# Performance work log

Measured on AMD Instinct MI355X. Metric: run time of the kernel, lower is better.

The kernel has to match this reference:

```python
import jax, jax.numpy as jnp
import numpy as np

H = W = 56
HID = 384
B = 16

def dct_mat(N):
    # Orthonormal DCT-II matrix: X = D @ x, idct via D.T
    n = jnp.arange(N, dtype=jnp.float32)
    k = jnp.arange(N, dtype=jnp.float32)[:, None]
    D = jnp.cos(jnp.pi * (2.0 * n + 1.0) * k / (2.0 * N)) * jnp.sqrt(2.0 / N)
    D = D.at[0].multiply(1.0 / jnp.sqrt(2.0))
    return D

def setup_inputs() -> dict:
    key = jax.random.key(0)
    ks = jax.random.split(key, 16)
    s = 0.02
    return {
        "x": jax.random.normal(ks[0], (B, HID, H, W), dtype=jnp.float32),
        "freq_embed": jax.random.normal(ks[1], (H, W, HID), dtype=jnp.float32),
        "dw_w": jax.random.normal(ks[2], (HID, 1, 3, 3), dtype=jnp.float32) * s,
        "dw_b": jnp.zeros((HID,), jnp.float32),
        "lin_w": jax.random.normal(ks[3], (2 * HID, HID), dtype=jnp.float32) * s,
        "lin_b": jnp.zeros((2 * HID,), jnp.float32),
        "vel_w": jax.random.normal(ks[4], (HID, HID), dtype=jnp.float32) * s,
        "vel_b": jnp.zeros((HID,), jnp.float32),
        "tok_w": jax.random.normal(ks[5], (HID, HID), dtype=jnp.float32) * s,
        "tok_b": jnp.zeros((HID,), jnp.float32),
        "ln_g": jnp.ones((HID,), jnp.float32),
        "ln_b": jnp.zeros((HID,), jnp.float32),
        "out_w": jax.random.normal(ks[6], (HID, HID), dtype=jnp.float32) * s,
        "out_b": jnp.zeros((HID,), jnp.float32),
        "c": jnp.ones((1,), jnp.float32),
        "alpha": jnp.ones((1,), jnp.float32) * 0.1,
    }

def reference(x, freq_embed, dw_w, dw_b, lin_w, lin_b, vel_w, vel_b,
              tok_w, tok_b, ln_g, ln_b, out_w, out_b, c, alpha):
    Bn, C, Hh, Ww = x.shape
    # depthwise 3x3 conv, padding=1
    x = jax.lax.conv_general_dilated(
        x, dw_w, (1, 1), 'SAME',
        dimension_numbers=('NCHW', 'OIHW', 'NCHW'),
        feature_group_count=C) + dw_b[None, :, None, None]
    xl = jnp.transpose(x, (0, 2, 3, 1))            # [B,H,W,C]
    xz = xl @ lin_w.T + lin_b                      # [B,H,W,2C]
    xg, z = jnp.split(xz, 2, axis=-1)
    DH, DW_ = dct_mat(Hh), dct_mat(Ww)
    x_ch = jnp.transpose(xg, (0, 3, 1, 2))         # [B,C,H,W]
    x_u0 = jnp.einsum('ih,jw,bchw->bcij', DH, DW_, x_ch)
    x_vel = xg @ vel_w.T + vel_b                   # [B,H,W,C]
    x_v0 = jnp.einsum('ih,jw,bchw->bcij', DH, DW_, jnp.transpose(x_vel, (0, 3, 1, 2)))
    # decay map exp(-(n^2+m^2)) on linspace(0,pi)
    wn = jnp.linspace(0.0, jnp.pi, Hh + 1)[:Hh][:, None]
    wm = jnp.linspace(0.0, jnp.pi, Ww + 1)[:Ww][None, :]
    decay = jnp.exp(-(wn ** 2 + wm ** 2))[None, None]
    x_u0 = x_u0 * decay
    x_v0 = x_v0 * decay
    # wave modulation from freq embedding (shared across batch)
    t = jax.nn.relu(freq_embed @ tok_w.T + tok_b)  # [H,W,C]
    t = jnp.transpose(t, (2, 0, 1))[None]          # [1,C,H,W]
    eps = 1e-6
    cos_t = jnp.cos(c[0] * t)
    sin_t = jnp.sin(c[0] * t) / (c[0] + eps)
    final = cos_t * x_u0 + sin_t * (x_v0 + 0.5 * alpha[0] * x_u0)
    x_final = jnp.einsum('hi,wj,bchw->bcij', DH, DW_, final)  # IDCT2D
    y = jnp.transpose(x_final, (0, 2, 3, 1))       # [B,H,W,C]
    mu = jnp.mean(y, axis=-1, keepdims=True)
    var = jnp.mean((y - mu) ** 2, axis=-1, keepdims=True)
    yn = (y - mu) / jnp.sqrt(var + 1e-5) * ln_g + ln_b
    gated = yn * jax.nn.silu(z)                    # [B,H,W,C]
    out = gated @ out_w.T + out_b
    return jnp.transpose(out, (0, 3, 1, 2))        # [B,C,H,W]
```

## Files before the change

### kernel.cpp

```cpp
#include <hip/hip_runtime.h>
#include <math.h>

#define HH 56
#define WS_W 56
#define HWS 3136
#define CD 384
#define BB 16
#define NROW (BB*HWS)
#define SLOT ((size_t)NROW*CD)

typedef __attribute__((ext_vector_type(8))) short bf16x8;
typedef __attribute__((ext_vector_type(4))) float f32x4;

__device__ inline ushort f2bf(float v) {
  uint u = __float_as_uint(v);
  uint r = (u + 0x7fffu + ((u >> 16) & 1u)) >> 16;
  return (ushort)r;
}
__device__ inline float bf2f(ushort h) { return __uint_as_float((uint)h << 16); }

__device__ inline void split_octet(const float* f, uint4& hi, uint4& lo) {
  ushort hs[8], ls[8];
  #pragma unroll
  for (int i = 0; i < 8; ++i) {
    float v = f[i];
    ushort h = f2bf(v);
    hs[i] = h;
    ls[i] = f2bf(v - bf2f(h));
  }
  hi.x = hs[0] | ((uint)hs[1] << 16); hi.y = hs[2] | ((uint)hs[3] << 16);
  hi.z = hs[4] | ((uint)hs[5] << 16); hi.w = hs[6] | ((uint)hs[7] << 16);
  lo.x = ls[0] | ((uint)ls[1] << 16); lo.y = ls[2] | ((uint)ls[3] << 16);
  lo.z = ls[4] | ((uint)ls[5] << 16); lo.w = ls[6] | ((uint)ls[7] << 16);
}

__global__ void prep_d_k(float* __restrict__ D) {
  for (int idx = threadIdx.x; idx < HH*HH; idx += blockDim.x) {
    int k = idx / HH, n = idx % HH;
    double v = cos(3.14159265358979323846 * (2.0*n + 1.0) * k / (2.0*HH)) * sqrt(2.0/HH);
    if (k == 0) v *= 0.70710678118654752440;
    D[idx] = (float)v;
  }
}

__global__ __launch_bounds__(256) void split_w_k(
    const float* __restrict__ W, ushort* __restrict__ hi,
    ushort* __restrict__ lo, int nelem) {
  int i = blockIdx.x*256 + threadIdx.x;
  if (i >= nelem) return;
  float v = W[i];
  ushort h = f2bf(v);
  hi[i] = h;
  lo[i] = f2bf(v - bf2f(h));
}

__global__ __launch_bounds__(256) void conv_k(
    const float* __restrict__ x, const float* __restrict__ dww,
    const float* __restrict__ dwb, float* __restrict__ xc)
{
  __shared__ float xs[3][58][33];
  __shared__ float wgt[32][9];
  __shared__ float wb[32];
  int t = threadIdx.x;
  int c0 = blockIdx.x * 32, h = blockIdx.y, b = blockIdx.z;
  for (int idx = t; idx < 1344; idx += 256) {
    int wq = idx % 14, rem = idx / 14;
    int dy = rem % 3, ch = rem / 3;
    int gh = h + dy - 1;
    float4 v = {0.f, 0.f, 0.f, 0.f};
    if (gh >= 0 && gh < HH)
      v = *(const float4*)(x + (((size_t)b*CD + c0 + ch)*HH + gh)*WS_W + wq*4);
    int wp = wq*4 + 1;
    xs[dy][wp+0][ch] = v.x;
    xs[dy][wp+1][ch] = v.y;
    xs[dy][wp+2][ch] = v.z;
    xs[dy][wp+3][ch] = v.w;
  }
  if (t < 192) {
    int e = t & 1, dy = (t >> 1) % 3, ch = t / 6;
    xs[dy][e*57][ch] = 0.f;
  }
  for (int idx = t; idx < 288; idx += 256)
    wgt[idx/9][idx%9] = dww[(size_t)(c0 + idx/9)*9 + idx%9];
  if (t < 32) wb[t] = dwb[c0 + t];
  __syncthreads();
  int ch = t & 31, wq8 = t >> 5;
  #pragma unroll
  for (int wwi = 0; wwi < 7; ++wwi) {
    int w = wwi*8 + wq8;
    float acc = wb[ch];
    #pragma unroll
    for (int dy = 0; dy < 3; ++dy)
      #pragma unroll
      for (int dx = 0; dx < 3; ++dx)
        acc = fmaf(wgt[ch][dy*3+dx], xs[dy][w+dx][ch], acc);
    xc[((size_t)b*HWS + h*WS_W + w)*CD + c0 + ch] = acc;
  }
}

template<int EPI>
__global__ __launch_bounds__(256) void gemm_k(
    const float* __restrict__ A, const float* __restrict__ Bw,
    const float* __restrict__ bias, float* __restrict__ out0,
    float* __restrict__ out1, const float* __restrict__ cptr)
{
  __shared__ float As[16][68];
  __shared__ float Bs[16][68];
  int t = threadIdx.x;
  int col0 = blockIdx.x * 64;
  int row0 = blockIdx.y * 64;
  int lr = t >> 2, lk = (t & 3) * 4;
  const float* Ap = A + (size_t)(row0 + lr)*CD + lk;
  const float* Bp = Bw + (size_t)(col0 + lr)*CD + lk;
  float acc[4][4] = {};
  int tx = t & 15, ty = t >> 4;
  for (int k0 = 0; k0 < CD; k0 += 16) {
    float4 av = *(const float4*)(Ap + k0);
    float4 bv = *(const float4*)(Bp + k0);
    __syncthreads();
    As[lk+0][lr] = av.x; As[lk+1][lr] = av.y; As[lk+2][lr] = av.z; As[lk+3][lr] = av.w;
    Bs[lk+0][lr] = bv.x; Bs[lk+1][lr] = bv.y; Bs[lk+2][lr] = bv.z; Bs[lk+3][lr] = bv.w;
    __syncthreads();
    #pragma unroll
    for (int k = 0; k < 16; ++k) {
      float4 a4 = *(const float4*)&As[k][ty*4];
      float4 b4 = *(const float4*)&Bs[k][tx*4];
      float aa[4] = {a4.x, a4.y, a4.z, a4.w};
      float bbv[4] = {b4.x, b4.y, b4.z, b4.w};
      #pragma unroll
      for (int i = 0; i < 4; ++i)
        #pragma unroll
        for (int j = 0; j < 4; ++j)
          acc[i][j] = fmaf(aa[i], bbv[j], acc[i][j]);
    }
  }
  float cs = 0.f;
  if constexpr (EPI == 2) cs = cptr[0];
  #pragma unroll
  for (int i = 0; i < 4; ++i) {
    int r = row0 + ty*4 + i;
    #pragma unroll
    for (int j = 0; j < 4; ++j) {
      int cg = col0 + tx*4 + j;
      float v = acc[i][j];
      if constexpr (EPI == 2) {
        v += bias[cg];
        v = fmaxf(v, 0.f);
        int pi = r / 56, pj = r % 56;
        float wn = 3.14159265358979323846f/56.f * (float)pi;
        float wm = 3.14159265358979323846f/56.f * (float)pj;
        float dec = expf(-(wn*wn + wm*wm));
        out0[(size_t)r*CD + cg] = cosf(cs*v)*dec;
        out1[(size_t)r*CD + cg] = sinf(cs*v)/(cs + 1e-6f)*dec;
      }
    }
  }
}

template<int EPI>
__global__ __launch_bounds__(256, 2) void mgemm_k(
    const float* __restrict__ A, const ushort* __restrict__ Wh,
    const ushort* __restrict__ Wl, const float* __restrict__ bias,
    float* __restrict__ out0, float* __restrict__ out1,
    const float* __restrict__ Uin, const float* __restrict__ cosD,
    const float* __restrict__ sinD, const float* __restrict__ velb,
    const float* __restrict__ alphap)
{
  __shared__ char smem[32768];
  int t = threadIdx.x;
  int col0 = blockIdx.x * 128, row0 = blockIdx.y * 128;
  int r = t >> 1, half = t & 1;
  int n = r & 15, rt = r >> 4, q0 = half * 2;
  const float*  Ap  = A  + (size_t)(row0 + r)*CD + half*16;
  const ushort* Bhp = Wh + (size_t)(col0 + r)*CD + half*16;
  const ushort* Blp = Wl + (size_t)(col0 + r)*CD + half*16;
  int aoff0 = rt*1024 + (q0*16 + n)*16;
  int aoff1 = rt*1024 + ((q0+1)*16 + n)*16;
  int boff0 = 16384 + aoff0, boff1 = 16384 + aoff1;
  int wid = t >> 6, lane = t & 63;
  int wr = wid >> 1, wc = wid & 1;
  f32x4 acc[4][4];
  #pragma unroll
  for (int i = 0; i < 4; ++i)
    #pragma unroll
    for (int j = 0; j < 4; ++j)
      acc[i][j] = (f32x4){0.f, 0.f, 0.f, 0.f};

  for (int k0 = 0; k0 < CD; k0 += 32) {
    float4 f0 = *(const float4*)(Ap + k0);
    float4 f1 = *(const float4*)(Ap + k0 + 4);
    float4 f2 = *(const float4*)(Ap + k0 + 8);
    float4 f3 = *(const float4*)(Ap + k0 + 12);
    uint4 bh0 = *(const uint4*)(Bhp + k0);
    uint4 bh1 = *(const uint4*)(Bhp + k0 + 8);
    uint4 bl0 = *(const uint4*)(Blp + k0);
    uint4 bl1 = *(const uint4*)(Blp + k0 + 8);
    __syncthreads();
    float fa[16] = {f0.x,f0.y,f0.z,f0.w, f1.x,f1.y,f1.z,f1.w,
                    f2.x,f2.y,f2.z,f2.w, f3.x,f3.y,f3.z,f3.w};
    uint4 ah0, al0, ah1, al1;
    split_octet(&fa[0], ah0, al0);
    split_octet(&fa[8], ah1, al1);
    *(uint4*)(smem + aoff0)        = ah0;
    *(uint4*)(smem + aoff0 + 8192) = al0;
    *(uint4*)(smem + aoff1)        = ah1;
    *(uint4*)(smem + aoff1 + 8192) = al1;
    *(uint4*)(smem + boff0)        = bh0;
    *(uint4*)(smem + boff0 + 8192) = bl0;
    *(uint4*)(smem + boff1)        = bh1;
    *(uint4*)(smem + boff1 + 8192) = bl1;
    __syncthreads();
    bf16x8 Ah[4], Al[4], Bh[4], Bl[4];
    #pragma unroll
    for (int i = 0; i < 4; ++i) {
      int ao = (wr*4 + i)*1024 + lane*16;
      Ah[i] = *(const bf16x8*)(smem + ao);
      Al[i] = *(const bf16x8*)(smem + ao + 8192);
      int bo = 16384 + (wc*4 + i)*1024 + lane*16;
      Bh[i] = *(const bf16x8*)(smem + bo);
      Bl[i] = *(const bf16x8*)(smem + bo + 8192);
    }
    #pragma unroll
    for (int i = 0; i < 4; ++i)
      #pragma unroll
      for (int j = 0; j < 4; ++j) {
        acc[i][j] = __builtin_amdgcn_mfma_f32_16x16x32_bf16(Ah[i], Bh[j], acc[i][j], 0, 0, 0);
        acc[i][j] = __builtin_amdgcn_mfma_f32_16x16x32_bf16(Ah[i], Bl[j], acc[i][j], 0, 0, 0);
        acc[i][j] = __builtin_amdgcn_mfma_f32_16x16x32_bf16(Al[i], Bh[j], acc[i][j], 0, 0, 0);
      }
  }

  int nn = lane & 15, qq = lane >> 4;
  float ahalf = 0.f;
  if constexpr (EPI == 1) ahalf = 0.5f * alphap[0];
  #pragma unroll
  for (int i = 0; i < 4; ++i) {
    #pragma unroll
    for (int j = 0; j < 4; ++j) {
      #pragma unroll
      for (int reg = 0; reg < 4; ++reg) {
        int rg = row0 + wr*64 + i*16 + qq*4 + reg;
        int cg = col0 + wc*64 + j*16 + nn;
        float v = acc[i][j][reg];
        if constexpr (EPI == 0) {
          v += bias[cg];
          if (cg < CD) out0[(size_t)rg*CD + cg] = v;
          else         out1[(size_t)rg*CD + cg - CD] = v;
        } else if constexpr (EPI == 1) {
          int p = rg % HWS;
          float u  = Uin[(size_t)rg*CD + cg];
          float cd = cosD[(size_t)p*CD + cg];
          float sd = sinD[(size_t)p*CD + cg];
          if (p == 0) v += 56.f * velb[cg];
          out0[(size_t)rg*CD + cg] = cd*u + sd*(v + ahalf*u);
        } else {
          v += bias[cg];
          int bidx = rg / HWS, hw = rg % HWS;
          out0[((size_t)bidx*CD + cg)*HWS + hw] = v;
        }
      }
    }
  }
}

__global__ __launch_bounds__(448) void dct_k(
    const float* __restrict__ in, float* __restrict__ out,
    const float* __restrict__ D, int NC, int trans)
{
  __shared__ float Ds[56][60];
  __shared__ float Xs[56][128];
  int t = threadIdx.x;
  int c0 = blockIdx.x * 128;
  size_t bt = blockIdx.y;
  for (int idx = t; idx < 3136; idx += 448) {
    int k = idx / 56, m = idx % 56;
    Ds[k][m] = trans ? D[k*56 + m] : D[m*56 + k];
  }
  const float* inb = in + bt*56*(size_t)NC + c0;
  for (int fi = t; fi < 56*32; fi += 448) {
    int rw = fi >> 5, cg = fi & 31;
    *(float4*)&Xs[rw][cg*4] = *(const float4*)(inb + (size_t)rw*NC + cg*4);
  }
  __syncthreads();
  int tx = t % 32, ty = t / 32;
  float acc[4][4] = {};
  #pragma unroll 4
  for (int k = 0; k < 56; ++k) {
    float4 a4 = *(const float4*)&Ds[k][ty*4];
    float4 b4 = *(const float4*)&Xs[k][tx*4];
    float aa[4] = {a4.x, a4.y, a4.z, a4.w};
    float bbv[4] = {b4.x, b4.y, b4.z, b4.w};
    #pragma unroll
    for (int i = 0; i < 4; ++i)
      #pragma unroll
      for (int j = 0; j < 4; ++j)
        acc[i][j] = fmaf(aa[i], bbv[j], acc[i][j]);
  }
  float* ob = out + bt*56*(size_t)NC + c0;
  #pragma unroll
  for (int i = 0; i < 4; ++i) {
    int m = ty*4 + i;
    float4 o; o.x = acc[i][0]; o.y = acc[i][1]; o.z = acc[i][2]; o.w = acc[i][3];
    *(float4*)(ob + (size_t)m*NC + tx*4) = o;
  }
}

__global__ __launch_bounds__(256) void ln_gate_k(
    const float* __restrict__ Y, const float* __restrict__ Z,
    const float* __restrict__ g, const float* __restrict__ be,
    float* __restrict__ out)
{
  int lane = threadIdx.x & 63, wv = threadIdx.x >> 6;
  size_t r = (size_t)blockIdx.x*4 + wv;
  const float* y = Y + r*CD;
  float v[6];
  float s = 0.f;
  #pragma unroll
  for (int q = 0; q < 6; ++q) { v[q] = y[lane + 64*q]; s += v[q]; }
  #pragma unroll
  for (int off = 32; off > 0; off >>= 1) s += __shfl_xor(s, off, 64);
  float mu = s * (1.f/384.f);
  float s2 = 0.f;
  #pragma unroll
  for (int q = 0; q < 6; ++q) { float d = v[q]-mu; s2 += d*d; }
  #pragma unroll
  for (int off = 32; off > 0; off >>= 1) s2 += __shfl_xor(s2, off, 64);
  float rs = 1.f / sqrtf(s2*(1.f/384.f) + 1e-5f);
  #pragma unroll
  for (int q = 0; q < 6; ++q) {
    int c = lane + 64*q;
    float yn = (v[q]-mu)*rs*g[c] + be[c];
    float zv = Z[r*CD + c];
    float sz = zv / (1.f + expf(-zv));
    out[r*CD + c] = yn*sz;
  }
}

extern "C" void kernel_launch(void* const* d_in, const int* in_sizes, int n_in,
                              void* d_out, int out_size, void* d_ws, size_t ws_size,
                              hipStream_t stream) {
  const float* x     = (const float*)d_in[0];
  const float* fe    = (const float*)d_in[1];
  const float* dw_w  = (const float*)d_in[2];
  const float* dw_b  = (const float*)d_in[3];
  const float* lin_w = (const float*)d_in[4];
  const float* lin_b = (const float*)d_in[5];
  const float* vel_w = (const float*)d_in[6];
  const float* vel_b = (const float*)d_in[7];
  const float* tok_w = (const float*)d_in[8];
  const float* tok_b = (const float*)d_in[9];
  const float* ln_g  = (const float*)d_in[10];
  const float* ln_b  = (const float*)d_in[11];
  const float* out_w = (const float*)d_in[12];
  const float* out_b = (const float*)d_in[13];
  const float* cp    = (const float*)d_in[14];
  const float* ap    = (const float*)d_in[15];

  float* ws    = (float*)d_ws;
  float* slotA = ws;
  float* slotB = ws + SLOT;
  float* slotC = ws + 2*SLOT;
  float* Dm    = ws + 3*SLOT;
  float* cosD  = Dm + 3136;
  float* sinD  = cosD + (size_t)HWS*CD;
  ushort* whi  = (ushort*)(sinD + (size_t)HWS*CD);
  ushort* wlo  = whi + 589824;

  prep_d_k<<<1, 256, 0, stream>>>(Dm);
  split_w_k<<<1152, 256, 0, stream>>>(lin_w, whi,          wlo,          294912);
  split_w_k<<< 576, 256, 0, stream>>>(vel_w, whi + 294912, wlo + 294912, 147456);
  split_w_k<<< 576, 256, 0, stream>>>(out_w, whi + 442368, wlo + 442368, 147456);

  conv_k<<<dim3(12, 56, 16), 256, 0, stream>>>(x, dw_w, dw_b, slotA);
  gemm_k<2><<<dim3(6, 49), 256, 0, stream>>>(fe, tok_w, tok_b, cosD, sinD, cp);
  mgemm_k<0><<<dim3(6, 392), 256, 0, stream>>>(slotA, whi, wlo, lin_b,
      slotB, slotC, nullptr, nullptr, nullptr, nullptr, nullptr);
  dct_k<<<dim3(168, 16), 448, 0, stream>>>(slotB, slotA, Dm, 21504, 0);
  dct_k<<<dim3(3, 896), 448, 0, stream>>>(slotA, slotB, Dm, 384, 0);
  mgemm_k<1><<<dim3(3, 392), 256, 0, stream>>>(slotB, whi + 294912, wlo + 294912,
      nullptr, slotA, nullptr, slotB, cosD, sinD, vel_b, ap);
  dct_k<<<dim3(168, 16), 448, 0, stream>>>(slotA, slotB, Dm, 21504, 1);
  dct_k<<<dim3(3, 896), 448, 0, stream>>>(slotB, slotA, Dm, 384, 1);
  ln_gate_k<<<12544, 256, 0, stream>>>(slotA, slotC, ln_g, ln_b, slotB);
  mgemm_k<3><<<dim3(3, 392), 256, 0, stream>>>(slotB, whi + 442368, wlo + 442368,
      out_b, (float*)d_out, nullptr, nullptr, nullptr, nullptr, nullptr, nullptr);
}
```

Measured before the change: 749.6 us.

## Emit bf16 hi/lo split activations from producer kernels instead of splitting in GEMM

The conv, second DCT pass and LayerNorm-gate kernels now write activations as pre-split bf16 hi/lo pairs. The MFMA GEMM then loads these directly into shared memory instead of converting fp32 on every K step. This removes redundant split arithmetic from the GEMM inner loop, since each A tile is re-split for every column block. It also raises the occupancy hint from 2 to 3 blocks per SM. Global traffic for A stays about the same (two 16-bit arrays replace one 32-bit array), and the split cost moves into the producer epilogues.

```diff
diff --git a/kernel.cpp b/kernel.cpp
--- a/kernel.cpp
+++ b/kernel.cpp
@@ -18,21 +18,6 @@
   return (ushort)r;
 }
 __device__ inline float bf2f(ushort h) { return __uint_as_float((uint)h << 16); }
-
-__device__ inline void split_octet(const float* f, uint4& hi, uint4& lo) {
-  ushort hs[8], ls[8];
-  #pragma unroll
-  for (int i = 0; i < 8; ++i) {
-    float v = f[i];
-    ushort h = f2bf(v);
-    hs[i] = h;
-    ls[i] = f2bf(v - bf2f(h));
-  }
-  hi.x = hs[0] | ((uint)hs[1] << 16); hi.y = hs[2] | ((uint)hs[3] << 16);
-  hi.z = hs[4] | ((uint)hs[5] << 16); hi.w = hs[6] | ((uint)hs[7] << 16);
-  lo.x = ls[0] | ((uint)ls[1] << 16); lo.y = ls[2] | ((uint)ls[3] << 16);
-  lo.z = ls[4] | ((uint)ls[5] << 16); lo.w = ls[6] | ((uint)ls[7] << 16);
-}
 
 __global__ void prep_d_k(float* __restrict__ D) {
   for (int idx = threadIdx.x; idx < HH*HH; idx += blockDim.x) {
@@ -56,7 +41,8 @@
 
 __global__ __launch_bounds__(256) void conv_k(
     const float* __restrict__ x, const float* __restrict__ dww,
-    const float* __restrict__ dwb, float* __restrict__ xc)
+    const float* __restrict__ dwb, ushort* __restrict__ xcH,
+    ushort* __restrict__ xcL)
 {
   __shared__ float xs[3][58][33];
   __shared__ float wgt[32][9];
@@ -94,7 +80,10 @@
       #pragma unroll
       for (int dx = 0; dx < 3; ++dx)
         acc = fmaf(wgt[ch][dy*3+dx], xs[dy][w+dx][ch], acc);
-    xc[((size_t)b*HWS + h*WS_W + w)*CD + c0 + ch] = acc;
+    size_t oi = ((size_t)b*HWS + h*WS_W + w)*CD + c0 + ch;
+    ushort hh = f2bf(acc);
+    xcH[oi] = hh;
+    xcL[oi] = f2bf(acc - bf2f(hh));
   }
 }
 
@@ -158,25 +147,26 @@
 }
 
 template<int EPI>
-__global__ __launch_bounds__(256, 2) void mgemm_k(
-    const float* __restrict__ A, const ushort* __restrict__ Wh,
-    const ushort* __restrict__ Wl, const float* __restrict__ bias,
+__global__ __launch_bounds__(256, 3) void mgemm_k(
+    const ushort* __restrict__ Ahg, const ushort* __restrict__ Alg,
+    const ushort* __restrict__ Wh, const ushort* __restrict__ Wl,
+    const float* __restrict__ bias,
     float* __restrict__ out0, float* __restrict__ out1,
-    const float* __restrict__ Uin, const float* __restrict__ cosD,
-    const float* __restrict__ sinD, const float* __restrict__ velb,
-    const float* __restrict__ alphap)
+    const ushort* __restrict__ UinH, const ushort* __restrict__ UinL,
+    const float* __restrict__ cosD, const float* __restrict__ sinD,
+    const float* __restrict__ velb, const float* __restrict__ alphap)
 {
   __shared__ char smem[32768];
   int t = threadIdx.x;
   int col0 = blockIdx.x * 128, row0 = blockIdx.y * 128;
   int r = t >> 1, half = t & 1;
-  int n = r & 15, rt = r >> 4, q0 = half * 2;
-  const float*  Ap  = A  + (size_t)(row0 + r)*CD + half*16;
-  const ushort* Bhp = Wh + (size_t)(col0 + r)*CD + half*16;
-  const ushort* Blp = Wl + (size_t)(col0 + r)*CD + half*16;
-  int aoff0 = rt*1024 + (q0*16 + n)*16;
-  int aoff1 = rt*1024 + ((q0+1)*16 + n)*16;
-  int boff0 = 16384 + aoff0, boff1 = 16384 + aoff1;
+  int n = r & 15, st = r >> 4, q0 = half * 2;
+  const ushort* Ahp = Ahg + (size_t)(row0 + r)*CD + half*16;
+  const ushort* Alp = Alg + (size_t)(row0 + r)*CD + half*16;
+  const ushort* Bhp = Wh  + (size_t)(col0 + r)*CD + half*16;
+  const ushort* Blp = Wl  + (size_t)(col0 + r)*CD + half*16;
+  int off0 = st*1024 + (q0*16 + n)*16;
+  int off1 = st*1024 + ((q0+1)*16 + n)*16;
   int wid = t >> 6, lane = t & 63;
   int wr = wid >> 1, wc = wid & 1;
   f32x4 acc[4][4];
@@ -187,28 +177,23 @@
       acc[i][j] = (f32x4){0.f, 0.f, 0.f, 0.f};
 
   for (int k0 = 0; k0 < CD; k0 += 32) {
-    float4 f0 = *(const float4*)(Ap + k0);
-    float4 f1 = *(const float4*)(Ap + k0 + 4);
-    float4 f2 = *(const float4*)(Ap + k0 + 8);
-    float4 f3 = *(const float4*)(Ap + k0 + 12);
-    uint4 bh0 = *(const uint4*)(Bhp + k0);
-    uint4 bh1 = *(const uint4*)(Bhp + k0 + 8);
-    uint4 bl0 = *(const uint4*)(Blp + k0);
-    uint4 bl1 = *(const uint4*)(Blp + k0 + 8);
+    uint4 a0 = *(const uint4*)(Ahp + k0);
+    uint4 a1 = *(const uint4*)(Ahp + k0 + 8);
+    uint4 l0 = *(const uint4*)(Alp + k0);
+    uint4 l1 = *(const uint4*)(Alp + k0 + 8);
+    uint4 b0 = *(const uint4*)(Bhp + k0);
+    uint4 b1 = *(const uint4*)(Bhp + k0 + 8);
+    uint4 c0v = *(const uint4*)(Blp + k0);
+    uint4 c1v = *(const uint4*)(Blp + k0 + 8);
     __syncthreads();
-    float fa[16] = {f0.x,f0.y,f0.z,f0.w, f1.x,f1.y,f1.z,f1.w,
-                    f2.x,f2.y,f2.z,f2.w, f3.x,f3.y,f3.z,f3.w};
-    uint4 ah0, al0, ah1, al1;
-    split_octet(&fa[0], ah0, al0);
-    split_octet(&fa[8], ah1, al1);
-    *(uint4*)(smem + aoff0)        = ah0;
-    *(uint4*)(smem + aoff0 + 8192) = al0;
-    *(uint4*)(smem + aoff1)        = ah1;
-    *(uint4*)(smem + aoff1 + 8192) = al1;
-    *(uint4*)(smem + boff0)        = bh0;
-    *(uint4*)(smem + boff0 + 8192) = bl0;
-    *(uint4*)(smem + boff1)        = bh1;
-    *(uint4*)(smem + boff1 + 8192) = bl1;
+    *(uint4*)(smem + off0)         = a0;
+    *(uint4*)(smem + off1)         = a1;
+    *(uint4*)(smem + off0 +  8192) = l0;
+    *(uint4*)(smem + off1 +  8192) = l1;
+    *(uint4*)(smem + off0 + 16384) = b0;
+    *(uint4*)(smem + off1 + 16384) = b1;
+    *(uint4*)(smem + off0 + 24576) = c0v;
+    *(uint4*)(smem + off1 + 24576) = c1v;
     __syncthreads();
     bf16x8 Ah[4], Al[4], Bh[4], Bl[4];
     #pragma unroll
@@ -248,11 +233,12 @@
           else         out1[(size_t)rg*CD + cg - CD] = v;
         } else if constexpr (EPI == 1) {
           int p = rg % HWS;
-          float u  = Uin[(size_t)rg*CD + cg];
+          size_t ui = (size_t)rg*CD + cg;
+          float u  = bf2f(UinH[ui]) + bf2f(UinL[ui]);
           float cd = cosD[(size_t)p*CD + cg];
           float sd = sinD[(size_t)p*CD + cg];
           if (p == 0) v += 56.f * velb[cg];
-          out0[(size_t)rg*CD + cg] = cd*u + sd*(v + ahalf*u);
+          out0[ui] = cd*u + sd*(v + ahalf*u);
         } else {
           v += bias[cg];
           int bidx = rg / HWS, hw = rg % HWS;
@@ -263,8 +249,10 @@
   }
 }
 
+template<int SPLIT>
 __global__ __launch_bounds__(448) void dct_k(
     const float* __restrict__ in, float* __restrict__ out,
+    ushort* __restrict__ outH, ushort* __restrict__ outL,
     const float* __restrict__ D, int NC, int trans)
 {
   __shared__ float Ds[56][60];
@@ -296,19 +284,30 @@
       for (int j = 0; j < 4; ++j)
         acc[i][j] = fmaf(aa[i], bbv[j], acc[i][j]);
   }
-  float* ob = out + bt*56*(size_t)NC + c0;
+  size_t obase = bt*56*(size_t)NC + c0;
   #pragma unroll
   for (int i = 0; i < 4; ++i) {
     int m = ty*4 + i;
-    float4 o; o.x = acc[i][0]; o.y = acc[i][1]; o.z = acc[i][2]; o.w = acc[i][3];
-    *(float4*)(ob + (size_t)m*NC + tx*4) = o;
+    if constexpr (SPLIT == 0) {
+      float4 o; o.x = acc[i][0]; o.y = acc[i][1]; o.z = acc[i][2]; o.w = acc[i][3];
+      *(float4*)(out + obase + (size_t)m*NC + tx*4) = o;
+    } else {
+      ushort4 oh, ol;
+      ushort h;
+      h = f2bf(acc[i][0]); oh.x = h; ol.x = f2bf(acc[i][0] - bf2f(h));
+      h = f2bf(acc[i][1]); oh.y = h; ol.y = f2bf(acc[i][1] - bf2f(h));
+      h = f2bf(acc[i][2]); oh.z = h; ol.z = f2bf(acc[i][2] - bf2f(h));
+      h = f2bf(acc[i][3]); oh.w = h; ol.w = f2bf(acc[i][3] - bf2f(h));
+      *(ushort4*)(outH + obase + (size_t)m*NC + tx*4) = oh;
+      *(ushort4*)(outL + obase + (size_t)m*NC + tx*4) = ol;
+    }
   }
 }
 
 __global__ __launch_bounds__(256) void ln_gate_k(
     const float* __restrict__ Y, const float* __restrict__ Z,
     const float* __restrict__ g, const float* __restrict__ be,
-    float* __restrict__ out)
+    ushort* __restrict__ outH, ushort* __restrict__ outL)
 {
   int lane = threadIdx.x & 63, wv = threadIdx.x >> 6;
   size_t r = (size_t)blockIdx.x*4 + wv;
@@ -332,7 +331,10 @@
     float yn = (v[q]-mu)*rs*g[c] + be[c];
     float zv = Z[r*CD + c];
     float sz = zv / (1.f + expf(-zv));
-    out[r*CD + c] = yn*sz;
+    float o = yn*sz;
+    ushort h = f2bf(o);
+    outH[r*CD + c] = h;
+    outL[r*CD + c] = f2bf(o - bf2f(h));
   }
 }
 
@@ -356,32 +358,36 @@
   const float* cp    = (const float*)d_in[14];
   const float* ap    = (const float*)d_in[15];
 
-  float* ws    = (float*)d_ws;
-  float* slotA = ws;
-  float* slotB = ws + SLOT;
-  float* slotC = ws + 2*SLOT;
+  float* ws = (float*)d_ws;
+  float* S0 = ws;
+  float* S1 = ws + SLOT;
+  float* S2 = ws + 2*SLOT;
   float* Dm    = ws + 3*SLOT;
   float* cosD  = Dm + 3136;
   float* sinD  = cosD + (size_t)HWS*CD;
   ushort* whi  = (ushort*)(sinD + (size_t)HWS*CD);
   ushort* wlo  = whi + 589824;
 
+  ushort* xcH = (ushort*)S0; ushort* xcL = xcH + SLOT;
+  ushort* UH  = (ushort*)S1; ushort* UL  = UH + SLOT;
+  ushort* GH  = (ushort*)S1; ushort* GL  = GH + SLOT;
+
   prep_d_k<<<1, 256, 0, stream>>>(Dm);
   split_w_k<<<1152, 256, 0, stream>>>(lin_w, whi,          wlo,          294912);
   split_w_k<<< 576, 256, 0, stream>>>(vel_w, whi + 294912, wlo + 294912, 147456);
   split_w_k<<< 576, 256, 0, stream>>>(out_w, whi + 442368, wlo + 442368, 147456);
 
-  conv_k<<<dim3(12, 56, 16), 256, 0, stream>>>(x, dw_w, dw_b, slotA);
+  conv_k<<<dim3(12, 56, 16), 256, 0, stream>>>(x, dw_w, dw_b, xcH, xcL);
   gemm_k<2><<<dim3(6, 49), 256, 0, stream>>>(fe, tok_w, tok_b, cosD, sinD, cp);
-  mgemm_k<0><<<dim3(6, 392), 256, 0, stream>>>(slotA, whi, wlo, lin_b,
-      slotB, slotC, nullptr, nullptr, nullptr, nullptr, nullptr);
-  dct_k<<<dim3(168, 16), 448, 0, stream>>>(slotB, slotA, Dm, 21504, 0);
-  dct_k<<<dim3(3, 896), 448, 0, stream>>>(slotA, slotB, Dm, 384, 0);
-  mgemm_k<1><<<dim3(3, 392), 256, 0, stream>>>(slotB, whi + 294912, wlo + 294912,
-      nullptr, slotA, nullptr, slotB, cosD, sinD, vel_b, ap);
-  dct_k<<<dim3(168, 16), 448, 0, stream>>>(slotA, slotB, Dm, 21504, 1);
-  dct_k<<<dim3(3, 896), 448, 0, stream>>>(slotB, slotA, Dm, 384, 1);
-  ln_gate_k<<<12544, 256, 0, stream>>>(slotA, slotC, ln_g, ln_b, slotB);
-  mgemm_k<3><<<dim3(3, 392), 256, 0, stream>>>(slotB, whi + 442368, wlo + 442368,
-      out_b, (float*)d_out, nullptr, nullptr, nullptr, nullptr, nullptr, nullptr);
-}
+  mgemm_k<0><<<dim3(6, 392), 256, 0, stream>>>(xcH, xcL, whi, wlo, lin_b,
+      S1, S2, nullptr, nullptr, nullptr, nullptr, nullptr, nullptr);
+  dct_k<0><<<dim3(168, 16), 448, 0, stream>>>(S1, S0, nullptr, nullptr, Dm, 21504, 0);
+  dct_k<1><<<dim3(3, 896), 448, 0, stream>>>(S0, nullptr, UH, UL, Dm, 384, 0);
+  mgemm_k<1><<<dim3(3, 392), 256, 0, stream>>>(UH, UL, whi + 294912, wlo + 294912,
+      nullptr, S0, nullptr, UH, UL, cosD, sinD, vel_b, ap);
+  dct_k<0><<<dim3(168, 16), 448, 0, stream>>>(S0, S1, nullptr, nullptr, Dm, 21504, 1);
+  dct_k<0><<<dim3(3, 896), 448, 0, stream>>>(S1, S0, nullptr, nullptr, Dm, 384, 1);
+  ln_gate_k<<<12544, 256, 0, stream>>>(S0, S2, ln_g, ln_b, GH, GL);
+  mgemm_k<3><<<dim3(3, 392), 256, 0, stream>>>(GH, GL, whi + 442368, wlo + 442368,
+      out_b, (float*)d_out, nullptr, nullptr, nullptr, nullptr, nullptr, nullptr, nullptr);
+}
```

After: 809.4 us. +8.0%, slower.
